# Performance work log

Measured on AMD Instinct MI355X. Metric: run time of the kernel, lower is better.

## Reference

```python
import jax, jax.numpy as jnp
import numpy as np
import math
from jax import lax

B, T, GS = 16, 511, 1
OBS, OUT = 60, 30
D, H, L = 1024, 16, 8
DFF, HID = 4096, 100
S = T + GS
DH = D // H
EPS = 1e-5


def _ln(x, g, b):
    m = jnp.mean(x, axis=-1, keepdims=True)
    v = jnp.mean(jnp.square(x - m), axis=-1, keepdims=True)
    return (x - m) * lax.rsqrt(v + EPS) * g + b


def setup_inputs():
    key = jax.random.key(0)
    ks = iter(jax.random.split(key, 32))
    def n(shape):
        return jax.random.normal(next(ks), shape, dtype=jnp.float32) * 0.02
    return {
        "states": jax.random.normal(next(ks), (B, T, OBS), dtype=jnp.float32),
        "goals": jax.random.normal(next(ks), (B, GS, OBS), dtype=jnp.float32),
        "Wtok": n((OBS, D)), "btok": jnp.zeros((D,), jnp.float32),
        "pos": n((1, S, D)),
        "ln1_g": jnp.ones((L, D), jnp.float32), "ln1_b": jnp.zeros((L, D), jnp.float32),
        "Wq": n((L, D, D)), "bq": jnp.zeros((L, D), jnp.float32),
        "Wk": n((L, D, D)), "bk": jnp.zeros((L, D), jnp.float32),
        "Wv": n((L, D, D)), "bv": jnp.zeros((L, D), jnp.float32),
        "Wp": n((L, D, D)), "bp": jnp.zeros((L, D), jnp.float32),
        "ln2_g": jnp.ones((L, D), jnp.float32), "ln2_b": jnp.zeros((L, D), jnp.float32),
        "Wm1": n((L, D, DFF)), "bm1": jnp.zeros((L, DFF), jnp.float32),
        "Wm2": n((L, DFF, D)), "bm2": jnp.zeros((L, D), jnp.float32),
        "lnf_g": jnp.ones((D,), jnp.float32), "lnf_b": jnp.zeros((D,), jnp.float32),
        "Wh1": n((D, HID)), "bh1": jnp.zeros((HID,), jnp.float32),
        "Wh2": n((HID, OUT)), "bh2": jnp.zeros((OUT,), jnp.float32),
    }


def reference(states, goals, Wtok, btok, pos, ln1_g, ln1_b, Wq, bq, Wk, bk, Wv, bv, Wp, bp,
              ln2_g, ln2_b, Wm1, bm1, Wm2, bm2, lnf_g, lnf_b, Wh1, bh1, Wh2, bh2):
    # token + positional embeddings (dropout is identity in eval mode, pdrop=0)
    goal_x = goals @ Wtok + btok + pos[:, :GS]
    state_x = states @ Wtok + btok + pos[:, GS:S]
    x = jnp.concatenate([goal_x, state_x], axis=1)  # (B, S, D)
    mask = jnp.tril(jnp.ones((S, S), dtype=bool))
    scale = 1.0 / math.sqrt(DH)

    def block(x, p):
        g1, b1, wq, bq_, wk, bk_, wv, bv_, wp, bp_, g2, b2, w1, bm1_, w2, bm2_ = p
        h = _ln(x, g1, b1)
        q = (h @ wq + bq_).reshape(B, S, H, DH).transpose(0, 2, 1, 3)  # (B,H,S,DH)
        k = (h @ wk + bk_).reshape(B, S, H, DH).transpose(0, 2, 1, 3)
        v = (h @ wv + bv_).reshape(B, S, H, DH).transpose(0, 2, 1, 3)
        att = jnp.einsum('bhqd,bhkd->bhqk', q, k) * scale
        att = jnp.where(mask, att, -jnp.inf)
        att = jax.nn.softmax(att, axis=-1)
        y = jnp.einsum('bhqk,bhkd->bhqd', att, v)
        y = y.transpose(0, 2, 1, 3).reshape(B, S, D) @ wp + bp_
        x = x + y
        h = _ln(x, g2, b2)
        x = x + (jax.nn.gelu(h @ w1 + bm1_, approximate=False) @ w2 + bm2_)
        return x, None

    x, _ = lax.scan(block, x, (ln1_g, ln1_b, Wq, bq, Wk, bk, Wv, bv, Wp, bp,
                               ln2_g, ln2_b, Wm1, bm1, Wm2, bm2))
    x = _ln(x, lnf_g, lnf_b)[:, GS:]  # drop goal tokens -> (B, T, D)
    h = jax.nn.silu(x @ Wh1 + bh1)
    return h @ Wh2 + bh2
```

## Files before the change

kernel.cpp:

```cpp
#include <hip/hip_runtime.h>
#include <cstdint>
#include <math.h>

#define NB_B   16
#define NB_T   511
#define NB_S   512
#define NB_OBS 60
#define NB_D   1024
#define NB_H   16
#define NB_L   8
#define NB_DFF 4096
#define NB_HID 100
#define NB_OUT 30
#define NB_M   8192
#define QKV_S  3072

typedef __attribute__((ext_vector_type(8))) short  short8;
typedef __attribute__((ext_vector_type(4))) short  short4v;
typedef __attribute__((ext_vector_type(4))) float  f32x4;
typedef __attribute__((ext_vector_type(8))) __bf16 bf16x8;

template <int N_> struct ic { static constexpr int v = N_; };

__device__ __forceinline__ short f2bf(float f) {
  union { float f; unsigned u; } a; a.f = f;
  unsigned u = a.u + 0x7fffu + ((a.u >> 16) & 1u);
  return (short)(u >> 16);
}

__device__ __forceinline__ void load_lds16(const void* g, void* l) {
  __builtin_amdgcn_global_load_lds(
      (__attribute__((address_space(1))) unsigned int*)(uintptr_t)g,
      (__attribute__((address_space(3))) unsigned int*)(unsigned)(uintptr_t)l,
      16, 0, 0);
}

__device__ __forceinline__ f32x4 mfma16(short8 a, short8 b, f32x4 c) {
  return __builtin_amdgcn_mfma_f32_16x16x32_bf16(
      __builtin_bit_cast(bf16x8, a), __builtin_bit_cast(bf16x8, b), c, 0, 0, 0);
}

__device__ __forceinline__ float gelu_fast(float v) {
  const float t = 1.5957691216057308f * (v + 0.044715f * v * v * v);
  const float e = __expf(fminf(t, 30.f));
  return v * (e / (e + 1.f));
}

__global__ __launch_bounds__(256) void tconv2_kernel(
    const float* __restrict__ src, short* __restrict__ dst,
    int R, int C, size_t sstride, size_t dstride) {
  __shared__ float t[64][65];
  const float* s0 = src + blockIdx.z * sstride;
  short* d0 = dst + blockIdx.z * dstride;
  const int c0 = blockIdx.x * 64, r0 = blockIdx.y * 64;
#pragma unroll
  for (int i = 0; i < 4; i++) {
    const int idx = threadIdx.x + i * 256;
    const int r = idx >> 4, c4 = (idx & 15) * 4;
    const float4 v = *(const float4*)&s0[(size_t)(r0 + r) * C + c0 + c4];
    t[r][c4 + 0] = v.x; t[r][c4 + 1] = v.y; t[r][c4 + 2] = v.z; t[r][c4 + 3] = v.w;
  }
  __syncthreads();
#pragma unroll
  for (int i = 0; i < 2; i++) {
    const int idx = threadIdx.x + i * 256;
    const int c = idx >> 3, g = (idx & 7) * 8;
    short8 o;
#pragma unroll
    for (int j = 0; j < 8; j++) o[j] = f2bf(t[g + j][c]);
    *(short8*)&d0[(size_t)(c0 + c) * R + r0 + g] = o;
  }
}

__global__ __launch_bounds__(256) void whead_prep(
    const float* __restrict__ Wh1, const float* __restrict__ bh1,
    short* __restrict__ Wh1t, float* __restrict__ bh1p) {
  const int idx = blockIdx.x * 256 + threadIdx.x;
  const int n = idx >> 10, k = idx & 1023;
  Wh1t[idx] = (n < NB_HID) ? f2bf(Wh1[k * NB_HID + n]) : (short)0;
  if (idx < 128) bh1p[idx] = (idx < NB_HID) ? bh1[idx] : 0.f;
}

__global__ __launch_bounds__(256) void qkvbias_prep(
    const float* __restrict__ bq, const float* __restrict__ bk,
    const float* __restrict__ bv, float* __restrict__ outb) {
  const int idx = blockIdx.x * 256 + threadIdx.x;
  const int l = idx / QKV_S, r = idx - l * QKV_S;
  const int z = r >> 10, c = r & 1023;
  const float* src = (z == 0) ? bq : ((z == 1) ? bk : bv);
  outb[idx] = src[l * NB_D + c];
}

__global__ __launch_bounds__(256) void embed2_kernel(
    const float* __restrict__ states, const float* __restrict__ goals,
    const float* __restrict__ Wtok, const float* __restrict__ btok,
    const float* __restrict__ pos, float* __restrict__ x) {
  const int r0 = blockIdx.x * 8;
  __shared__ float tok[8][NB_OBS];
  for (int idx = threadIdx.x; idx < 8 * NB_OBS; idx += 256) {
    const int r = idx / NB_OBS, o = idx - r * NB_OBS;
    const int row = r0 + r, b = row >> 9, s = row & 511;
    tok[r][o] = (s == 0) ? goals[b * NB_OBS + o]
                         : states[((size_t)b * NB_T + (s - 1)) * NB_OBS + o];
  }
  __syncthreads();
#pragma unroll
  for (int i = 0; i < 4; i++) {
    const int d = threadIdx.x + i * 256;
    float acc[8];
#pragma unroll
    for (int r = 0; r < 8; r++) acc[r] = 0.f;
    for (int o = 0; o < NB_OBS; o++) {
      const float wv = Wtok[o * NB_D + d];
#pragma unroll
      for (int r = 0; r < 8; r++) acc[r] += tok[r][o] * wv;
    }
    const float bt = btok[d];
#pragma unroll
    for (int r = 0; r < 8; r++) {
      const int row = r0 + r, s = row & 511;
      x[(size_t)row * NB_D + d] = acc[r] + bt + pos[(size_t)s * NB_D + d];
    }
  }
}

template <typename OutT>
__global__ __launch_bounds__(256) void ln_wave(
    const float* __restrict__ xin, const float* __restrict__ gam,
    const float* __restrict__ bet, OutT* __restrict__ outp) {
  const int row = blockIdx.x * 4 + (threadIdx.x >> 6);
  const int lane = threadIdx.x & 63;
  const float4* src = (const float4*)(xin + (size_t)row * NB_D);
  float4 v[4];
  float s = 0.f, s2 = 0.f;
#pragma unroll
  for (int i = 0; i < 4; i++) {
    v[i] = src[lane + 64 * i];
    s += v[i].x + v[i].y + v[i].z + v[i].w;
    s2 += v[i].x * v[i].x + v[i].y * v[i].y + v[i].z * v[i].z + v[i].w * v[i].w;
  }
#pragma unroll
  for (int o = 32; o; o >>= 1) {
    s += __shfl_xor(s, o, 64);
    s2 += __shfl_xor(s2, o, 64);
  }
  const float mean = s * (1.f / NB_D);
  const float var = s2 * (1.f / NB_D) - mean * mean;
  const float rs = rsqrtf(var + 1e-5f);
#pragma unroll
  for (int i = 0; i < 4; i++) {
    const float4 g4 = ((const float4*)gam)[lane + 64 * i];
    const float4 b4 = ((const float4*)bet)[lane + 64 * i];
    const float o0 = (v[i].x - mean) * rs * g4.x + b4.x;
    const float o1 = (v[i].y - mean) * rs * g4.y + b4.y;
    const float o2 = (v[i].z - mean) * rs * g4.z + b4.z;
    const float o3 = (v[i].w - mean) * rs * g4.w + b4.w;
    if constexpr (sizeof(OutT) == 2) {
      short4v r = {f2bf(o0), f2bf(o1), f2bf(o2), f2bf(o3)};
      *(short4v*)((short*)outp + (size_t)row * NB_D + (lane + 64 * i) * 4) = r;
    } else {
      ((float4*)((float*)outp + (size_t)row * NB_D))[lane + 64 * i] =
          make_float4(o0, o1, o2, o3);
    }
  }
}

template <int BM, int N, int K, int ACT, bool RESID, typename OutT>
__device__ __forceinline__ void gemmv4_core(
    const short* __restrict__ A, const short* __restrict__ Bt,
    const float* __restrict__ bias, const float* __restrict__ resid,
    OutT* __restrict__ C) {
  constexpr int MI = BM / 32;
  constexpr int NK = K / 32;
  constexpr int NBN = N / 128;
  constexpr int NWG = (NB_M / BM) * NBN;
  constexpr int QC = NWG / 8;
  constexpr int L = 2 + BM / 64;
  constexpr int SA = BM * 32;

  __shared__ short As[3][SA];
  __shared__ short Bs[3][128 * 32];

  int wg = blockIdx.x;
  wg = (wg & 7) * QC + (wg >> 3);
  const int bm = (wg / NBN) * BM;
  const int bn = (wg % NBN) * 128;

  const int tid = threadIdx.x;
  const int w = tid >> 6, lane = tid & 63;
  const int wm = w >> 1, wn = w & 1;
  const int rr = lane & 15, sg = lane >> 4;
  const int lrow = lane >> 2, lslot = lane & 3;
  const int sslot = lslot ^ ((lrow >> 1) & 3);

  const short* Asrc = A + (size_t)(bm + w * 16 + lrow) * K + sslot * 8;
  const short* Bsrc = Bt + (size_t)(bn + w * 16 + lrow) * K + sslot * 8;
  short* Adst = &As[0][w * 512];
  short* Bdst = &Bs[0][w * 512];

  const int ar = wm * (BM / 2) + rr;
  const int br = wn * 64 + rr;
  const int aoff = ar * 32 + ((sg ^ ((ar >> 1) & 3)) * 8);
  const int boff = br * 32 + ((sg ^ ((br >> 1) & 3)) * 8);

  f32x4 acc[MI][4];
#pragma unroll
  for (int i = 0; i < MI; i++)
#pragma unroll
    for (int j = 0; j < 4; j++) acc[i][j] = f32x4{0.f, 0.f, 0.f, 0.f};

  auto stage = [&](int sb, int k0) {
    load_lds16(Bsrc + k0,                  Bdst + sb * 4096);
    load_lds16(Bsrc + (size_t)64 * K + k0, Bdst + sb * 4096 + 2048);
#pragma unroll
    for (int c = 0; c < BM / 64; c++)
      load_lds16(Asrc + (size_t)(c * 64) * K + k0, Adst + sb * SA + c * 2048);
  };

  auto gate = [&]() {
    if constexpr (L == 6) asm volatile("s_waitcnt vmcnt(6)" ::: "memory");
    else                  asm volatile("s_waitcnt vmcnt(4)" ::: "memory");
  };

  stage(0, 0);
  stage(1, 32);
  gate();
  __builtin_amdgcn_s_barrier();

  auto ktile = [&](auto BUFC, auto SBUFC, int t) {
    constexpr int BUF = decltype(BUFC)::v;
    constexpr int SBUF = decltype(SBUFC)::v;
    const short* Ab = &As[BUF][0];
    const short* Bb = &Bs[BUF][0];
    if (t + 2 < NK) stage(SBUF, (t + 2) * 32);
    short8 a[MI], b[4];
#pragma unroll
    for (int i = 0; i < MI; i++) a[i] = *(const short8*)(Ab + aoff + i * 512);
#pragma unroll
    for (int j = 0; j < 4; j++) b[j] = *(const short8*)(Bb + boff + j * 512);
    __builtin_amdgcn_s_setprio(1);
#pragma unroll
    for (int i = 0; i < MI; i++)
#pragma unroll
      for (int j = 0; j < 4; j++) acc[i][j] = mfma16(a[i], b[j], acc[i][j]);
    __builtin_amdgcn_s_setprio(0);
    if (t + 2 < NK)      gate();
    else if (t + 1 < NK) asm volatile("s_waitcnt vmcnt(0)" ::: "memory");
    __builtin_amdgcn_s_barrier();
  };

  int t = 0;
#pragma unroll 1
  for (; t + 3 <= NK; t += 3) {
    ktile(ic<0>{}, ic<2>{}, t);
    ktile(ic<1>{}, ic<0>{}, t + 1);
    ktile(ic<2>{}, ic<1>{}, t + 2);
  }
  if constexpr (NK % 3 >= 1) ktile(ic<0>{}, ic<2>{}, NK - NK % 3);
  if constexpr (NK % 3 >= 2) ktile(ic<1>{}, ic<0>{}, NK - NK % 3 + 1);

  const int col0 = bn + wn * 64 + rr;
  float bv[4];
#pragma unroll
  for (int j = 0; j < 4; j++) bv[j] = bias[col0 + j * 16];
#pragma unroll
  for (int i = 0; i < MI; i++) {
#pragma unroll
    for (int q = 0; q < 4; q++) {
      const size_t row = bm + wm * (BM / 2) + i * 16 + sg * 4 + q;
      float v0 = acc[i][0][q] + bv[0];
      float v1 = acc[i][1][q] + bv[1];
      float v2 = acc[i][2][q] + bv[2];
      float v3 = acc[i][3][q] + bv[3];
      if constexpr (RESID) {
        const float* rrow = resid + row * N + col0;
        v0 += rrow[0]; v1 += rrow[16]; v2 += rrow[32]; v3 += rrow[48];
      }
      if constexpr (ACT == 1) {
        v0 = gelu_fast(v0); v1 = gelu_fast(v1);
        v2 = gelu_fast(v2); v3 = gelu_fast(v3);
      }
      OutT* crow = C + row * N + col0;
      if constexpr (sizeof(OutT) == 2) {
        crow[0] = (OutT)f2bf(v0); crow[16] = (OutT)f2bf(v1);
        crow[32] = (OutT)f2bf(v2); crow[48] = (OutT)f2bf(v3);
      } else {
        crow[0] = v0; crow[16] = v1; crow[32] = v2; crow[48] = v3;
      }
    }
  }
}

template <int BM, int N, int K, int ACT, bool RESID, typename OutT>
__global__ __launch_bounds__(256, 2) void gemmv4(
    const short* __restrict__ A, const short* __restrict__ Bt,
    const float* __restrict__ bias, const float* __restrict__ resid,
    OutT* __restrict__ C) {
  gemmv4_core<BM, N, K, ACT, RESID, OutT>(A, Bt, bias, resid, C);
}

template <int ACT, bool RESID, typename OutT>
__global__ __launch_bounds__(256) void gemm_bt(
    const short* __restrict__ A, const short* __restrict__ Bt,
    const float* __restrict__ bias, const float* __restrict__ resid,
    OutT* __restrict__ C, int N, int K) {
  __shared__ short As[128][32];
  __shared__ short Bs[128][32];
  const int bm = blockIdx.y * 128, bn = blockIdx.x * 128;
  const int tid = threadIdx.x;
  const int w = tid >> 6, lane = tid & 63;
  const int wr = (w >> 1) * 64, wc = (w & 1) * 64;
  const int rr = lane & 15, sg = lane >> 4;

  f32x4 acc[4][4];
#pragma unroll
  for (int i = 0; i < 4; i++)
#pragma unroll
    for (int j = 0; j < 4; j++) acc[i][j] = f32x4{0.f, 0.f, 0.f, 0.f};

  const int srow0 = w * 32 + (lane >> 2);
  const int sslot = lane & 3;

  for (int k0 = 0; k0 < K; k0 += 32) {
    __syncthreads();
#pragma unroll
    for (int inst = 0; inst < 2; inst++) {
      const int r = srow0 + inst * 16;
      const int sl = sslot ^ ((r >> 1) & 3);
      load_lds16(A + (size_t)(bm + r) * K + k0 + sl * 8, &As[w * 32 + inst * 16][0]);
      load_lds16(Bt + (size_t)(bn + r) * K + k0 + sl * 8, &Bs[w * 32 + inst * 16][0]);
    }
    __syncthreads();
    short8 a[4], b[4];
#pragma unroll
    for (int i = 0; i < 4; i++) {
      const int r = wr + i * 16 + rr;
      a[i] = *(const short8*)&As[r][(sg ^ ((r >> 1) & 3)) * 8];
      const int c = wc + i * 16 + rr;
      b[i] = *(const short8*)&Bs[c][(sg ^ ((c >> 1) & 3)) * 8];
    }
#pragma unroll
    for (int i = 0; i < 4; i++)
#pragma unroll
      for (int j = 0; j < 4; j++) acc[i][j] = mfma16(a[i], b[j], acc[i][j]);
  }

#pragma unroll
  for (int j = 0; j < 4; j++) {
    const int col = bn + wc + j * 16 + rr;
    const float bv = bias[col];
#pragma unroll
    for (int i = 0; i < 4; i++) {
#pragma unroll
      for (int q = 0; q < 4; q++) {
        const int row = bm + wr + i * 16 + sg * 4 + q;
        float v = acc[i][j][q] + bv;
        if constexpr (RESID) v += resid[(size_t)row * N + col];
        if constexpr (ACT == 1) v = gelu_fast(v);
        if constexpr (ACT == 2) v = v / (1.f + __expf(-v));
        if constexpr (sizeof(OutT) == 2) C[(size_t)row * N + col] = (OutT)f2bf(v);
        else C[(size_t)row * N + col] = v;
      }
    }
  }
}

__global__ __launch_bounds__(256) void attn2_kernel(
    const short* __restrict__ qkv, short* __restrict__ out) {
  const int qt = blockIdx.x, hh = blockIdx.y, bb = blockIdx.z;
  const int tid = threadIdx.x;
  const int w = tid >> 6, lane = tid & 63;
  const int rr = lane & 15, sg = lane >> 4;

  __shared__ short Ks[64][64];
  __shared__ short Vt[64][64];
  __shared__ short Ps[4][16][64];

  const int qrow_base = qt * 128 + w * 32;

  short8 qf[2][2];
#pragma unroll
  for (int g = 0; g < 2; g++) {
    const size_t qrow = (size_t)bb * NB_S + qrow_base + g * 16 + rr;
#pragma unroll
    for (int ks = 0; ks < 2; ks++)
      qf[g][ks] = *(const short8*)&qkv[qrow * QKV_S + hh * 64 + ks * 32 + sg * 8];
  }

  float mrow[2][4], lrow[2][4];
  f32x4 o[2][4];
#pragma unroll
  for (int g = 0; g < 2; g++)
#pragma unroll
    for (int j = 0; j < 4; j++) {
      mrow[g][j] = -INFINITY; lrow[g][j] = 0.f;
      o[g][j] = f32x4{0.f, 0.f, 0.f, 0.f};
    }

  const int ktmax = 2 * qt + 1;
  for (int kt = 0; kt <= ktmax; kt++) {
    __syncthreads();
    {
      const int p = lane & 7;
#pragma unroll
      for (int inst = 0; inst < 2; inst++) {
        const int r = w * 16 + inst * 8 + (lane >> 3);
        const int sl = p ^ (r & 7);
        load_lds16(qkv + ((size_t)bb * NB_S + kt * 64 + r) * QKV_S + 1024 + hh * 64 + sl * 8,
                   &Ks[w * 16 + inst * 8][0]);
      }
    }
    {
#pragma unroll
      for (int cc = 0; cc < 2; cc++) {
        const int c = tid * 2 + cc;
        const int sk = c >> 3, sl = c & 7;
        short8 vv = *(const short8*)&qkv[((size_t)bb * NB_S + kt * 64 + sk) * QKV_S + 2048 + hh * 64 + sl * 8];
        const int ss = sk >> 3;
#pragma unroll
        for (int j = 0; j < 8; j++) {
          const int dh = sl * 8 + j;
          Vt[dh][(ss ^ (dh & 7)) * 8 + (sk & 7)] = vv[j];
        }
      }
    }
    __syncthreads();

#pragma unroll
    for (int g = 0; g < 2; g++) {
      if (kt * 64 > qrow_base + g * 16 + 15) continue;

      f32x4 sf[4];
#pragma unroll
      for (int nb = 0; nb < 4; nb++) sf[nb] = f32x4{0.f, 0.f, 0.f, 0.f};
#pragma unroll
      for (int ks = 0; ks < 2; ks++) {
#pragma unroll
        for (int nb = 0; nb < 4; nb++) {
          const int ck = nb * 16 + rr;
          short8 kf = *(const short8*)&Ks[ck][((ks * 4 + sg) ^ (ck & 7)) * 8];
          sf[nb] = mfma16(qf[g][ks], kf, sf[nb]);
        }
      }
      const int rbase = qrow_base + g * 16 + sg * 4;
      float pmax[4] = {-INFINITY, -INFINITY, -INFINITY, -INFINITY};
#pragma unroll
      for (int nb = 0; nb < 4; nb++) {
        const int cg = kt * 64 + nb * 16 + rr;
#pragma unroll
        for (int j = 0; j < 4; j++) {
          float sv = sf[nb][j] * 0.125f;
          if (cg > rbase + j) sv = -INFINITY;
          sf[nb][j] = sv;
          pmax[j] = fmaxf(pmax[j], sv);
        }
      }
#pragma unroll
      for (int o1 = 1; o1 < 16; o1 <<= 1)
#pragma unroll
        for (int j = 0; j < 4; j++)
          pmax[j] = fmaxf(pmax[j], __shfl_xor(pmax[j], o1, 64));

      float resc[4], psum[4];
#pragma unroll
      for (int j = 0; j < 4; j++) {
        const float mn = fmaxf(mrow[g][j], pmax[j]);
        resc[j] = __expf(mrow[g][j] - mn);
        mrow[g][j] = mn;
        psum[j] = 0.f;
      }
#pragma unroll
      for (int nb = 0; nb < 4; nb++)
#pragma unroll
        for (int j = 0; j < 4; j++) {
          const float p = __expf(sf[nb][j] - mrow[g][j]);
          sf[nb][j] = p;
          psum[j] += p;
        }
#pragma unroll
      for (int o1 = 1; o1 < 16; o1 <<= 1)
#pragma unroll
        for (int j = 0; j < 4; j++) psum[j] += __shfl_xor(psum[j], o1, 64);
#pragma unroll
      for (int j = 0; j < 4; j++) lrow[g][j] = lrow[g][j] * resc[j] + psum[j];
#pragma unroll
      for (int nb = 0; nb < 4; nb++)
#pragma unroll
        for (int j = 0; j < 4; j++) o[g][nb][j] *= resc[j];

#pragma unroll
      for (int nb = 0; nb < 4; nb++) {
        const int ck = nb * 16 + rr;
        const int ss = ck >> 3;
#pragma unroll
        for (int j = 0; j < 4; j++) {
          const int rq = sg * 4 + j;
          Ps[w][rq][(ss ^ (rq & 7)) * 8 + (ck & 7)] = f2bf(sf[nb][j]);
        }
      }
#pragma unroll
      for (int ks = 0; ks < 2; ks++) {
        short8 pf = *(const short8*)&Ps[w][rr][((ks * 4 + sg) ^ (rr & 7)) * 8];
#pragma unroll
        for (int nb = 0; nb < 4; nb++) {
          const int dh = nb * 16 + rr;
          short8 vf = *(const short8*)&Vt[dh][((ks * 4 + sg) ^ (dh & 7)) * 8];
          o[g][nb] = mfma16(pf, vf, o[g][nb]);
        }
      }
    }
  }

#pragma unroll
  for (int g = 0; g < 2; g++) {
    const size_t orow0 = (size_t)bb * NB_S + qrow_base + g * 16;
#pragma unroll
    for (int nb = 0; nb < 4; nb++)
#pragma unroll
      for (int j = 0; j < 4; j++) {
        const float v = o[g][nb][j] / lrow[g][j];
        out[(orow0 + sg * 4 + j) * NB_D + hh * 64 + nb * 16 + rr] = f2bf(v);
      }
  }
}

__global__ __launch_bounds__(256) void head2_kernel(
    const float* __restrict__ hbuf, const float* __restrict__ Wh2,
    const float* __restrict__ bh2, float* __restrict__ outp) {
  __shared__ float hs[8][NB_HID];
  const int g0 = blockIdx.x * 8;
  for (int idx = threadIdx.x; idx < 8 * NB_HID; idx += 256) {
    const int r = idx / NB_HID, k = idx - r * NB_HID;
    const int gt = g0 + r;
    const int b = gt / NB_T, tt = gt - b * NB_T;
    hs[r][k] = hbuf[(size_t)(b * NB_S + 1 + tt) * 128 + k];
  }
  __syncthreads();
  const int r = threadIdx.x >> 5, c = threadIdx.x & 31;
  if (c < NB_OUT) {
    float acc = bh2[c];
#pragma unroll
    for (int k = 0; k < NB_HID; k++) acc += hs[r][k] * Wh2[k * NB_OUT + c];
    outp[(size_t)(g0 + r) * NB_OUT + c] = acc;
  }
}

extern "C" void kernel_launch(void* const* d_in, const int* in_sizes, int n_in,
                              void* d_out, int out_size, void* d_ws, size_t ws_size,
                              hipStream_t stream) {
  const float* states = (const float*)d_in[0];
  const float* goals  = (const float*)d_in[1];
  const float* Wtok   = (const float*)d_in[2];
  const float* btok   = (const float*)d_in[3];
  const float* pos    = (const float*)d_in[4];
  const float* ln1_g  = (const float*)d_in[5];
  const float* ln1_b  = (const float*)d_in[6];
  const float* Wq     = (const float*)d_in[7];
  const float* bq     = (const float*)d_in[8];
  const float* Wk     = (const float*)d_in[9];
  const float* bk     = (const float*)d_in[10];
  const float* Wv     = (const float*)d_in[11];
  const float* bv     = (const float*)d_in[12];
  const float* Wp     = (const float*)d_in[13];
  const float* bp     = (const float*)d_in[14];
  const float* ln2_g  = (const float*)d_in[15];
  const float* ln2_b  = (const float*)d_in[16];
  const float* Wm1    = (const float*)d_in[17];
  const float* bm1    = (const float*)d_in[18];
  const float* Wm2    = (const float*)d_in[19];
  const float* bm2    = (const float*)d_in[20];
  const float* lnf_g  = (const float*)d_in[21];
  const float* lnf_b  = (const float*)d_in[22];
  const float* Wh1    = (const float*)d_in[23];
  const float* bh1    = (const float*)d_in[24];
  const float* Wh2    = (const float*)d_in[25];
  const float* bh2    = (const float*)d_in[26];

  char* wsp = (char*)d_ws;
  size_t off = 0;
  auto carve = [&](size_t bytes) -> char* {
    char* p = wsp + off;
    off += (bytes + 1023) & ~(size_t)1023;
    return p;
  };
  short* Wqkv_t = (short*)carve((size_t)NB_L * 3 * NB_D * NB_D * 2);
  short* Wp_t   = (short*)carve((size_t)NB_L * NB_D * NB_D * 2);
  short* Wm1_t  = (short*)carve((size_t)NB_L * NB_DFF * NB_D * 2);
  short* Wm2_t  = (short*)carve((size_t)NB_L * NB_D * NB_DFF * 2);
  float* x      = (float*)carve((size_t)NB_M * NB_D * 4);
  short* h      = (short*)carve((size_t)NB_M * NB_D * 2);
  short* qkvb   = (short*)carve((size_t)NB_M * QKV_S * 2);
  short* mlp    = (short*)carve((size_t)NB_M * NB_DFF * 2);
  short* Wh1t   = (short*)carve((size_t)128 * NB_D * 2);
  float* bh1p   = (float*)carve(128 * 4);
  float* bqkv   = (float*)carve((size_t)NB_L * QKV_S * 4);
  short* attout = mlp;
  float* hbuf   = (float*)qkvb;

  const dim3 thr(256);
  const size_t DD = (size_t)NB_D * NB_D;
  const size_t DF = (size_t)NB_D * NB_DFF;

  tconv2_kernel<<<dim3(16, 16, NB_L), thr, 0, stream>>>(Wq, Wqkv_t + 0 * DD, NB_D, NB_D, DD, 3 * DD);
  tconv2_kernel<<<dim3(16, 16, NB_L), thr, 0, stream>>>(Wk, Wqkv_t + 1 * DD, NB_D, NB_D, DD, 3 * DD);
  tconv2_kernel<<<dim3(16, 16, NB_L), thr, 0, stream>>>(Wv, Wqkv_t + 2 * DD, NB_D, NB_D, DD, 3 * DD);
  tconv2_kernel<<<dim3(16, 16, NB_L), thr, 0, stream>>>(Wp, Wp_t, NB_D, NB_D, DD, DD);
  tconv2_kernel<<<dim3(64, 16, NB_L), thr, 0, stream>>>(Wm1, Wm1_t, NB_D, NB_DFF, DF, DF);
  tconv2_kernel<<<dim3(16, 64, NB_L), thr, 0, stream>>>(Wm2, Wm2_t, NB_DFF, NB_D, DF, DF);
  whead_prep<<<512, thr, 0, stream>>>(Wh1, bh1, Wh1t, bh1p);
  qkvbias_prep<<<96, thr, 0, stream>>>(bq, bk, bv, bqkv);

  embed2_kernel<<<NB_M / 8, thr, 0, stream>>>(states, goals, Wtok, btok, pos, x);

  for (int l = 0; l < NB_L; l++) {
    ln_wave<short><<<NB_M / 4, thr, 0, stream>>>(x, ln1_g + l * NB_D, ln1_b + l * NB_D, h);
    gemmv4<256, QKV_S, NB_D, 0, false, short><<<768, thr, 0, stream>>>(
        h, Wqkv_t + (size_t)l * 3 * DD, bqkv + (size_t)l * QKV_S, nullptr, qkvb);
    attn2_kernel<<<dim3(NB_S / 128, NB_H, NB_B), thr, 0, stream>>>(qkvb, attout);
    gemmv4<128, NB_D, NB_D, 0, true, float><<<512, thr, 0, stream>>>(
        attout, Wp_t + (size_t)l * DD, bp + l * NB_D, x, x);
    ln_wave<short><<<NB_M / 4, thr, 0, stream>>>(x, ln2_g + l * NB_D, ln2_b + l * NB_D, h);
    gemmv4<256, NB_DFF, NB_D, 1, false, short><<<1024, thr, 0, stream>>>(
        h, Wm1_t + (size_t)l * DF, bm1 + l * NB_DFF, nullptr, mlp);
    gemmv4<128, NB_D, NB_DFF, 0, true, float><<<512, thr, 0, stream>>>(
        mlp, Wm2_t + (size_t)l * DF, bm2 + l * NB_D, x, x);
  }

  ln_wave<short><<<NB_M / 4, thr, 0, stream>>>(x, lnf_g, lnf_b, h);
  gemm_bt<2, false, float><<<dim3(1, NB_M / 128), thr, 0, stream>>>(
      h, Wh1t, bh1p, nullptr, hbuf, 128, NB_D);
  head2_kernel<<<NB_M / 8, thr, 0, stream>>>(hbuf, Wh2, bh2, (float*)d_out);
}
```

Baseline: 2.844 ms.

## Compute softmax row sums via MFMA with ones and group GEMM tile swizzle

In the attention kernel, the per-row softmax denominator is now computed by an extra MFMA of the bf16 probabilities against a vector of ones. This replaces the scalar accumulation and the four-step cross-lane shuffle reduction. The sum is therefore taken over the bf16-rounded probabilities, which matches what feeds the PV product but changes numerics slightly. Separately, the GEMM workgroup-to-tile mapping is regrouped into blocks of up to 8 column tiles per row chunk, aiming for better L2 reuse.

```diff
diff --git a/kernel.cpp b/kernel.cpp
--- a/kernel.cpp
+++ b/kernel.cpp
@@ -175,6 +175,8 @@
   constexpr int NBN = N / 128;
   constexpr int NWG = (NB_M / BM) * NBN;
   constexpr int QC = NWG / 8;
+  constexpr int CBM = QC / NBN;
+  constexpr int GN = (NBN < 8) ? NBN : 8;
   constexpr int L = 2 + BM / 64;
   constexpr int SA = BM * 32;
 
@@ -183,8 +185,12 @@
 
   int wg = blockIdx.x;
   wg = (wg & 7) * QC + (wg >> 3);
-  const int bm = (wg / NBN) * BM;
-  const int bn = (wg % NBN) * 128;
+  const int chunk = wg / QC;
+  const int idx = wg - chunk * QC;
+  const int grp = idx / (CBM * GN);
+  const int r2 = idx - grp * (CBM * GN);
+  const int bm = (chunk * CBM + r2 / GN) * BM;
+  const int bn = (grp * GN + r2 % GN) * 128;
 
   const int tid = threadIdx.x;
   const int w = tid >> 6, lane = tid & 63;
@@ -376,6 +382,9 @@
   __shared__ short Vt[64][64];
   __shared__ short Ps[4][16][64];
 
+  const short ONEB = 0x3F80;
+  const short8 ones8 = {ONEB, ONEB, ONEB, ONEB, ONEB, ONEB, ONEB, ONEB};
+
   const int qrow_base = qt * 128 + w * 32;
 
   short8 qf[2][2];
@@ -461,28 +470,18 @@
         for (int j = 0; j < 4; j++)
           pmax[j] = fmaxf(pmax[j], __shfl_xor(pmax[j], o1, 64));
 
-      float resc[4], psum[4];
+      float resc[4];
 #pragma unroll
       for (int j = 0; j < 4; j++) {
         const float mn = fmaxf(mrow[g][j], pmax[j]);
         resc[j] = __expf(mrow[g][j] - mn);
         mrow[g][j] = mn;
-        psum[j] = 0.f;
       }
 #pragma unroll
       for (int nb = 0; nb < 4; nb++)
 #pragma unroll
-        for (int j = 0; j < 4; j++) {
-          const float p = __expf(sf[nb][j] - mrow[g][j]);
-          sf[nb][j] = p;
-          psum[j] += p;
-        }
-#pragma unroll
-      for (int o1 = 1; o1 < 16; o1 <<= 1)
-#pragma unroll
-        for (int j = 0; j < 4; j++) psum[j] += __shfl_xor(psum[j], o1, 64);
-#pragma unroll
-      for (int j = 0; j < 4; j++) lrow[g][j] = lrow[g][j] * resc[j] + psum[j];
+        for (int j = 0; j < 4; j++)
+          sf[nb][j] = __expf(sf[nb][j] - mrow[g][j]);
 #pragma unroll
       for (int nb = 0; nb < 4; nb++)
 #pragma unroll
@@ -498,9 +497,11 @@
           Ps[w][rq][(ss ^ (rq & 7)) * 8 + (ck & 7)] = f2bf(sf[nb][j]);
         }
       }
+      f32x4 lacc = f32x4{0.f, 0.f, 0.f, 0.f};
 #pragma unroll
       for (int ks = 0; ks < 2; ks++) {
         short8 pf = *(const short8*)&Ps[w][rr][((ks * 4 + sg) ^ (rr & 7)) * 8];
+        lacc = mfma16(pf, ones8, lacc);
 #pragma unroll
         for (int nb = 0; nb < 4; nb++) {
           const int dh = nb * 16 + rr;
@@ -508,6 +509,8 @@
           o[g][nb] = mfma16(pf, vf, o[g][nb]);
         }
       }
+#pragma unroll
+      for (int j = 0; j < 4; j++) lrow[g][j] = lrow[g][j] * resc[j] + lacc[j];
     }
   }
 
```

Result: no change. 2.811 ms (-1.2%).
